# Kernel optimization log

Measured on AMD Instinct MI355X. Metric: run time of the kernel, lower is better.

The kernel has to match this reference:

```python
import jax, jax.numpy as jnp
import numpy as np

N, D, H = 8192, 256, 128
KEEP_RATIO = 0.5
TEMP = 1.0
COS_EPS = 1e-4  # torch CosineSimilarity eps
NEG = -9e15


def setup_inputs() -> dict:
    key = jax.random.key(0)
    k1, k2, k3, k4 = jax.random.split(key, 4)
    features = jax.random.normal(k1, (N, D), dtype=jnp.float32)
    adj = jax.random.randint(k2, (N, N), 0, 2, dtype=jnp.int32)
    # module init: Linear weights ~ N(0, 0.001)
    Wq = jax.random.normal(k3, (H, D), dtype=jnp.float32) * 0.001
    Wk = jax.random.normal(k4, (H, D), dtype=jnp.float32) * 0.001
    return {"features": features, "adj": adj, "Wq": Wq, "Wk": Wk}


def _cos_normalize(x):
    # torch cosine: x / max(||x||, eps)
    n = jnp.linalg.norm(x, axis=-1, keepdims=True)
    return x / jnp.maximum(n, COS_EPS)


def reference(features, adj, Wq, Wk):
    # projections [N, H]
    Qn = _cos_normalize(features @ Wq.T)
    Kn = _cos_normalize(features @ Wk.T)
    # raw_att[i, j] = cos(Wq f_j, Wk f_i)  -> [N, N]
    raw_att = Kn @ Qn.T
    att = jnp.where(adj > 0, raw_att, NEG) * TEMP
    att = jax.nn.softmax(att, axis=1)
    prop_fea = att @ features  # [N, D]
    # nodes with no neighbors keep their own features
    adj_mask = (jnp.sum(adj, axis=1) > 0).astype(features.dtype)[:, None]
    prop_fea = adj_mask * prop_fea + (1.0 - adj_mask) * features
    # gate=None branch: fixed keep_ratio mixing
    return (1.0 - KEEP_RATIO) * prop_fea + KEEP_RATIO * features
```

## Files before the change

kernel.cpp:

```cpp
#include <hip/hip_runtime.h>
#include <stdint.h>
#include <stddef.h>

#define NN 8192
#define DD 256
#define HH 128

typedef short bf16x8  __attribute__((ext_vector_type(8)));
typedef float f32x4   __attribute__((ext_vector_type(4)));
typedef float f32x16  __attribute__((ext_vector_type(16)));
typedef int   i32x4   __attribute__((ext_vector_type(4)));

static __device__ __forceinline__ short f2bf(float x){
  unsigned u = __float_as_uint(x);
  u = (u + 0x7FFFu + ((u >> 16) & 1u)) >> 16;
  return (short)(unsigned short)u;
}
static __device__ __forceinline__ bf16x8 cvt8(const float* p){
  f32x4 a = *(const f32x4*)p;
  f32x4 b = *(const f32x4*)(p + 4);
  bf16x8 o;
  o[0]=f2bf(a[0]); o[1]=f2bf(a[1]); o[2]=f2bf(a[2]); o[3]=f2bf(a[3]);
  o[4]=f2bf(b[0]); o[5]=f2bf(b[1]); o[6]=f2bf(b[2]); o[7]=f2bf(b[3]);
  return o;
}
static __device__ __forceinline__ bf16x8 ld16(const void* p){
  i32x4 v = *(const i32x4*)p;
  return __builtin_bit_cast(bf16x8, v);
}

__global__ __launch_bounds__(256) void k_prep(const float* __restrict__ f,
                                              const float* __restrict__ Wq,
                                              const float* __restrict__ Wk,
                                              unsigned short* __restrict__ ftf,
                                              unsigned short* __restrict__ Qnf,
                                              unsigned short* __restrict__ Kn){
  __shared__ unsigned short wb[128][40];
  int t = threadIdx.x, l = t & 63;
  {
    int fr = blockIdx.x * 4 + (t >> 6);
    int jt = fr >> 3, dt = fr & 7;
    int j = jt * 16 + (l >> 5) * 8, d = dt * 32 + (l & 31);
    bf16x8 o;
    #pragma unroll
    for (int e = 0; e < 8; ++e) o[e] = f2bf(f[(size_t)(j + e) * DD + d]);
    *(bf16x8*)(ftf + (size_t)fr * 512 + l * 8) = o;
  }
  if (blockIdx.x >= 128) return;
  int wave = t >> 6;
  int i0 = blockIdx.x * 64 + wave * 16;
  int lr = l & 15, lk = l >> 4;
  bf16x8 ka[8];
  #pragma unroll
  for (int ks = 0; ks < 8; ++ks)
    ka[ks] = cvt8(f + (size_t)(i0 + lr) * DD + ks * 32 + lk * 8);
  for (int pj = 0; pj < 2; ++pj){
    const float* W = pj ? Wk : Wq;
    f32x4 acc[8];
    #pragma unroll
    for (int n = 0; n < 8; ++n) acc[n] = (f32x4){0.f,0.f,0.f,0.f};
    for (int ks = 0; ks < 8; ++ks){
      __syncthreads();
      { int row = t >> 1, c0 = (t & 1) * 16;
        const float* wp = W + (size_t)row * DD + ks * 32 + c0;
        bf16x8 w0 = cvt8(wp), w1 = cvt8(wp + 8);
        *(bf16x8*)&wb[row][c0]     = w0;
        *(bf16x8*)&wb[row][c0 + 8] = w1; }
      __syncthreads();
      #pragma unroll
      for (int n = 0; n < 8; ++n){
        bf16x8 bb = ld16(&wb[n * 16 + lr][lk * 8]);
        acc[n] = __builtin_amdgcn_mfma_f32_16x16x32_bf16(ka[ks], bb, acc[n], 0, 0, 0);
      }
    }
    #pragma unroll
    for (int r = 0; r < 4; ++r){
      float n2 = 0.f;
      #pragma unroll
      for (int n = 0; n < 8; ++n){ float v = acc[n][r]; n2 += v * v; }
      n2 += __shfl_xor(n2, 1); n2 += __shfl_xor(n2, 2);
      n2 += __shfl_xor(n2, 4); n2 += __shfl_xor(n2, 8);
      float s = 1.f / fmaxf(sqrtf(n2), 1e-4f);
      int row = i0 + lk * 4 + r;
      #pragma unroll
      for (int n = 0; n < 8; ++n){
        short v = f2bf(acc[n][r] * s);
        if (pj){
          Kn[(size_t)row * HH + n * 16 + lr] = (unsigned short)v;
        } else {
          size_t off = ((size_t)(row >> 5) * 8 + n) * 512
                     + ((row & 31) + 32 * (lr >> 3)) * 8 + (lr & 7);
          Qnf[off] = (unsigned short)v;
        }
      }
    }
  }
}

__global__ __launch_bounds__(256, 2) void k_attn(
      const int* __restrict__ adj,
      const unsigned short* __restrict__ Qnf, const unsigned short* __restrict__ Kn,
      const unsigned short* __restrict__ ftf,
      float* __restrict__ num_p, float* __restrict__ den_p){
  __shared__ __attribute__((aligned(16))) char p_lds[8192];
  __shared__ __attribute__((aligned(16))) int adj_lds[2][64][64];
  int t = threadIdx.x, wave = t >> 6, l = t & 63;
  int lc = l & 31, h = l >> 5;
  int ig = wave >> 1, jg = wave & 1, wq = wave;
  int ib = blockIdx.x >> 2, js = blockIdx.x & 3;
  int i0 = ib * 64;
  int jbase = js * 2048;

  bf16x8 kb[8];
  { const unsigned short* kp = Kn + (size_t)(i0 + ig * 32 + lc) * HH + h * 8;
    #pragma unroll
    for (int hs = 0; hs < 8; ++hs) kb[hs] = ld16(kp + hs * 16); }

  f32x16 pv00, pv01, pv10, pv11;
  #pragma unroll
  for (int e = 0; e < 16; ++e){ pv00[e]=0.f; pv01[e]=0.f; pv10[e]=0.f; pv11[e]=0.f; }
  float dacc[16];
  #pragma unroll
  for (int r = 0; r < 16; ++r) dacc[r] = 0.f;

  int arow = wave * 16 + (l >> 4);
  int acol = (l & 15) * 4;

  #pragma unroll
  for (int k4 = 0; k4 < 4; ++k4){
    i32x4 v = __builtin_nontemporal_load(
        (const i32x4*)(adj + (size_t)(i0 + arow + k4 * 4) * NN + jbase + acol));
    *(i32x4*)&adj_lds[0][arow + k4 * 4][acol] = v;
  }
  __syncthreads();

  for (int s = 0; s < 32; ++s){
    int j0 = jbase + s * 64;
    int cur = s & 1, nxt = cur ^ 1;

    i32x4 av[4];
    if (s < 31){
      #pragma unroll
      for (int k4 = 0; k4 < 4; ++k4)
        av[k4] = __builtin_nontemporal_load(
            (const i32x4*)(adj + (size_t)(i0 + arow + k4 * 4) * NN + j0 + 64 + acol));
    }

    bf16x8 qv[8];
    { const unsigned short* qb = Qnf + ((size_t)((j0 + jg * 32) >> 5) * 8) * 512 + (size_t)l * 8;
      #pragma unroll
      for (int hs = 0; hs < 8; ++hs) qv[hs] = ld16(qb + hs * 512); }

    bf16x8 bv[8];
    { const unsigned short* fb = ftf + ((size_t)(j0 >> 4) * 8 + wq * 2) * 512 + (size_t)l * 8;
      #pragma unroll
      for (int ks = 0; ks < 4; ++ks){
        bv[ks * 2]     = ld16(fb + ks * 4096);
        bv[ks * 2 + 1] = ld16(fb + ks * 4096 + 512); } }

    f32x16 st;
    #pragma unroll
    for (int e = 0; e < 16; ++e) st[e] = 0.f;
    #pragma unroll
    for (int hs = 0; hs < 8; ++hs)
      st = __builtin_amdgcn_mfma_f32_32x32x16_bf16(kb[hs], qv[hs], st, 0, 0, 0);

    #pragma unroll
    for (int r = 0; r < 16; ++r){
      int row = ig * 32 + (r & 3) + 8 * (r >> 2) + 4 * h;
      int a = adj_lds[cur][row][jg * 32 + lc];
      float wv = (a > 0) ? __expf(st[r]) : 0.f;
      dacc[r] += wv;
      int byo = row * 128 + (((jg * 32 + lc) * 2) ^ ((row & 7) << 4));
      *(unsigned short*)(p_lds + byo) = (unsigned short)f2bf(wv);
    }
    __syncthreads();

    if (s < 31){
      #pragma unroll
      for (int k4 = 0; k4 < 4; ++k4)
        *(i32x4*)&adj_lds[nxt][arow + k4 * 4][acol] = av[k4];
    }

    #pragma unroll
    for (int ks = 0; ks < 4; ++ks){
      int ko = (ks * 32 + h * 16) ^ ((lc & 7) << 4);
      bf16x8 pa0 = ld16(p_lds + lc * 128 + ko);
      bf16x8 pa1 = ld16(p_lds + (32 + lc) * 128 + ko);
      pv00 = __builtin_amdgcn_mfma_f32_32x32x16_bf16(pa0, bv[ks*2],   pv00, 0,0,0);
      pv01 = __builtin_amdgcn_mfma_f32_32x32x16_bf16(pa0, bv[ks*2+1], pv01, 0,0,0);
      pv10 = __builtin_amdgcn_mfma_f32_32x32x16_bf16(pa1, bv[ks*2],   pv10, 0,0,0);
      pv11 = __builtin_amdgcn_mfma_f32_32x32x16_bf16(pa1, bv[ks*2+1], pv11, 0,0,0);
    }
    __syncthreads();
  }

  #pragma unroll
  for (int r = 0; r < 16; ++r){
    float v = dacc[r];
    v += __shfl_xor(v, 1); v += __shfl_xor(v, 2); v += __shfl_xor(v, 4);
    v += __shfl_xor(v, 8); v += __shfl_xor(v, 16);
    if (lc == 0){
      int i = i0 + ig * 32 + (r & 3) + 8 * (r >> 2) + 4 * h;
      den_p[(size_t)(js * 2 + jg) * NN + i] = v;
    }
  }
  float* np = num_p + (size_t)js * NN * DD;
  #pragma unroll
  for (int r = 0; r < 16; ++r){
    int i = i0 + (r & 3) + 8 * (r >> 2) + 4 * h;
    int d = wq * 64 + lc;
    np[(size_t)i * DD + d]             = pv00[r];
    np[(size_t)i * DD + d + 32]        = pv01[r];
    np[(size_t)(i + 32) * DD + d]      = pv10[r];
    np[(size_t)(i + 32) * DD + d + 32] = pv11[r];
  }
}

__global__ __launch_bounds__(256) void k_final(const float* __restrict__ num_p,
                                               const float* __restrict__ den_p,
                                               const float* __restrict__ f,
                                               float* __restrict__ out){
  int gid = blockIdx.x * 256 + threadIdx.x;
  int i = gid >> 6;
  f32x4 nv = (f32x4){0.f,0.f,0.f,0.f};
  float dv = 0.f;
  #pragma unroll
  for (int s = 0; s < 4; ++s)
    nv += *(const f32x4*)(num_p + (size_t)s * NN * DD + (size_t)gid * 4);
  #pragma unroll
  for (int s = 0; s < 8; ++s)
    dv += den_p[(size_t)s * NN + i];
  f32x4 fv = *(const f32x4*)(f + (size_t)gid * 4);
  f32x4 o;
  if (dv > 0.f){
    float inv = 0.5f / dv;
    o = nv * inv + fv * 0.5f;
  } else {
    o = fv;
  }
  *(f32x4*)(out + (size_t)gid * 4) = o;
}

extern "C" void kernel_launch(void* const* d_in, const int* in_sizes, int n_in,
                              void* d_out, int out_size, void* d_ws, size_t ws_size,
                              hipStream_t stream){
  (void)in_sizes; (void)n_in; (void)out_size;
  const float* feat = (const float*)d_in[0];
  const int*   adj  = (const int*)d_in[1];
  const float* Wq   = (const float*)d_in[2];
  const float* Wk   = (const float*)d_in[3];
  float* out = (float*)d_out;
  char* ws = (char*)d_ws;
  unsigned short* Qnf  = (unsigned short*)(ws);
  unsigned short* Kn   = (unsigned short*)(ws + (2u << 20));
  unsigned short* ftf  = (unsigned short*)(ws + (4u << 20));
  float*          num_p = (float*)(ws + (8u << 20));
  float*          den_p = (float*)(ws + (40u << 20));
  if (ws_size < (40u << 20) + 262144u) return;

  k_prep<<<1024, 256, 0, stream>>>(feat, Wq, Wk, ftf, Qnf, Kn);
  k_attn<<<512, 256, 0, stream>>>(adj, Qnf, Kn, ftf, num_p, den_p);
  k_final<<<2048, 256, 0, stream>>>(num_p, den_p, feat, out);
}
```

Baseline: 193.2 us.

## Fuse prep, attention and final kernels into one cooperative persistent kernel

Merges the three kernels into one phase-switched kernel launched cooperatively with 512 blocks, separated by grid-wide syncs. The prep and final phases are remapped so that each block covers more work to fit the 512-block grid. The aim is to remove two kernel launch gaps and their tail effects. In exchange it adds grid-sync cost and requires 512 blocks to be co-resident (two per CU on 256 CUs); if the cooperative launch fails, it falls back to three launches.

```diff
diff --git a/kernel.cpp b/kernel.cpp
--- a/kernel.cpp
+++ b/kernel.cpp
@@ -1,10 +1,13 @@
 #include <hip/hip_runtime.h>
+#include <hip/hip_cooperative_groups.h>
 #include <stdint.h>
 #include <stddef.h>
 
 #define NN 8192
 #define DD 256
 #define HH 128
+
+namespace cg = cooperative_groups;
 
 typedef short bf16x8  __attribute__((ext_vector_type(8)));
 typedef float f32x4   __attribute__((ext_vector_type(4)));
@@ -29,217 +32,220 @@
   return __builtin_bit_cast(bf16x8, v);
 }
 
-__global__ __launch_bounds__(256) void k_prep(const float* __restrict__ f,
-                                              const float* __restrict__ Wq,
-                                              const float* __restrict__ Wk,
-                                              unsigned short* __restrict__ ftf,
-                                              unsigned short* __restrict__ Qnf,
-                                              unsigned short* __restrict__ Kn){
+__global__ __launch_bounds__(256, 2) void k_mega(
+    const float* __restrict__ f, const int* __restrict__ adj,
+    const float* __restrict__ Wq, const float* __restrict__ Wk,
+    unsigned short* __restrict__ ftf, unsigned short* __restrict__ Qnf,
+    unsigned short* __restrict__ Kn,
+    float* __restrict__ num_p, float* __restrict__ den_p,
+    float* __restrict__ out, int phase)
+{
   __shared__ unsigned short wb[128][40];
-  int t = threadIdx.x, l = t & 63;
-  {
-    int fr = blockIdx.x * 4 + (t >> 6);
-    int jt = fr >> 3, dt = fr & 7;
-    int j = jt * 16 + (l >> 5) * 8, d = dt * 32 + (l & 31);
-    bf16x8 o;
-    #pragma unroll
-    for (int e = 0; e < 8; ++e) o[e] = f2bf(f[(size_t)(j + e) * DD + d]);
-    *(bf16x8*)(ftf + (size_t)fr * 512 + l * 8) = o;
-  }
-  if (blockIdx.x >= 128) return;
-  int wave = t >> 6;
-  int i0 = blockIdx.x * 64 + wave * 16;
-  int lr = l & 15, lk = l >> 4;
-  bf16x8 ka[8];
-  #pragma unroll
-  for (int ks = 0; ks < 8; ++ks)
-    ka[ks] = cvt8(f + (size_t)(i0 + lr) * DD + ks * 32 + lk * 8);
-  for (int pj = 0; pj < 2; ++pj){
-    const float* W = pj ? Wk : Wq;
-    f32x4 acc[8];
-    #pragma unroll
-    for (int n = 0; n < 8; ++n) acc[n] = (f32x4){0.f,0.f,0.f,0.f};
-    for (int ks = 0; ks < 8; ++ks){
-      __syncthreads();
-      { int row = t >> 1, c0 = (t & 1) * 16;
-        const float* wp = W + (size_t)row * DD + ks * 32 + c0;
-        bf16x8 w0 = cvt8(wp), w1 = cvt8(wp + 8);
-        *(bf16x8*)&wb[row][c0]     = w0;
-        *(bf16x8*)&wb[row][c0 + 8] = w1; }
-      __syncthreads();
-      #pragma unroll
-      for (int n = 0; n < 8; ++n){
-        bf16x8 bb = ld16(&wb[n * 16 + lr][lk * 8]);
-        acc[n] = __builtin_amdgcn_mfma_f32_16x16x32_bf16(ka[ks], bb, acc[n], 0, 0, 0);
-      }
-    }
-    #pragma unroll
-    for (int r = 0; r < 4; ++r){
-      float n2 = 0.f;
-      #pragma unroll
-      for (int n = 0; n < 8; ++n){ float v = acc[n][r]; n2 += v * v; }
-      n2 += __shfl_xor(n2, 1); n2 += __shfl_xor(n2, 2);
-      n2 += __shfl_xor(n2, 4); n2 += __shfl_xor(n2, 8);
-      float s = 1.f / fmaxf(sqrtf(n2), 1e-4f);
-      int row = i0 + lk * 4 + r;
-      #pragma unroll
-      for (int n = 0; n < 8; ++n){
-        short v = f2bf(acc[n][r] * s);
-        if (pj){
-          Kn[(size_t)row * HH + n * 16 + lr] = (unsigned short)v;
-        } else {
-          size_t off = ((size_t)(row >> 5) * 8 + n) * 512
-                     + ((row & 31) + 32 * (lr >> 3)) * 8 + (lr & 7);
-          Qnf[off] = (unsigned short)v;
-        }
-      }
-    }
-  }
-}
-
-__global__ __launch_bounds__(256, 2) void k_attn(
-      const int* __restrict__ adj,
-      const unsigned short* __restrict__ Qnf, const unsigned short* __restrict__ Kn,
-      const unsigned short* __restrict__ ftf,
-      float* __restrict__ num_p, float* __restrict__ den_p){
   __shared__ __attribute__((aligned(16))) char p_lds[8192];
   __shared__ __attribute__((aligned(16))) int adj_lds[2][64][64];
-  int t = threadIdx.x, wave = t >> 6, l = t & 63;
-  int lc = l & 31, h = l >> 5;
-  int ig = wave >> 1, jg = wave & 1, wq = wave;
-  int ib = blockIdx.x >> 2, js = blockIdx.x & 3;
-  int i0 = ib * 64;
-  int jbase = js * 2048;
-
-  bf16x8 kb[8];
-  { const unsigned short* kp = Kn + (size_t)(i0 + ig * 32 + lc) * HH + h * 8;
-    #pragma unroll
-    for (int hs = 0; hs < 8; ++hs) kb[hs] = ld16(kp + hs * 16); }
-
-  f32x16 pv00, pv01, pv10, pv11;
+  int bid = blockIdx.x, t = threadIdx.x, wave = t >> 6, l = t & 63;
+
+  if (phase <= 0){
+    #pragma unroll
+    for (int sub = 0; sub < 2; ++sub){
+      int fr = bid * 8 + wave * 2 + sub;
+      int jt = fr >> 3, dt = fr & 7;
+      int j = jt * 16 + (l >> 5) * 8, d = dt * 32 + (l & 31);
+      bf16x8 o;
+      #pragma unroll
+      for (int e = 0; e < 8; ++e) o[e] = f2bf(f[(size_t)(j + e) * DD + d]);
+      *(bf16x8*)(ftf + (size_t)fr * 512 + l * 8) = o;
+    }
+    if (bid < 128){
+      int i0 = bid * 64 + wave * 16;
+      int lr = l & 15, lk = l >> 4;
+      bf16x8 ka[8];
+      #pragma unroll
+      for (int ks = 0; ks < 8; ++ks)
+        ka[ks] = cvt8(f + (size_t)(i0 + lr) * DD + ks * 32 + lk * 8);
+      for (int pj = 0; pj < 2; ++pj){
+        const float* W = pj ? Wk : Wq;
+        f32x4 acc[8];
+        #pragma unroll
+        for (int n = 0; n < 8; ++n) acc[n] = (f32x4){0.f,0.f,0.f,0.f};
+        for (int ks = 0; ks < 8; ++ks){
+          __syncthreads();
+          { int row = t >> 1, c0 = (t & 1) * 16;
+            const float* wp = W + (size_t)row * DD + ks * 32 + c0;
+            bf16x8 w0 = cvt8(wp), w1 = cvt8(wp + 8);
+            *(bf16x8*)&wb[row][c0]     = w0;
+            *(bf16x8*)&wb[row][c0 + 8] = w1; }
+          __syncthreads();
+          #pragma unroll
+          for (int n = 0; n < 8; ++n){
+            bf16x8 bb = ld16(&wb[n * 16 + lr][lk * 8]);
+            acc[n] = __builtin_amdgcn_mfma_f32_16x16x32_bf16(ka[ks], bb, acc[n], 0, 0, 0);
+          }
+        }
+        #pragma unroll
+        for (int r = 0; r < 4; ++r){
+          float n2 = 0.f;
+          #pragma unroll
+          for (int n = 0; n < 8; ++n){ float v = acc[n][r]; n2 += v * v; }
+          n2 += __shfl_xor(n2, 1); n2 += __shfl_xor(n2, 2);
+          n2 += __shfl_xor(n2, 4); n2 += __shfl_xor(n2, 8);
+          float s = 1.f / fmaxf(sqrtf(n2), 1e-4f);
+          int row = i0 + lk * 4 + r;
+          #pragma unroll
+          for (int n = 0; n < 8; ++n){
+            short v = f2bf(acc[n][r] * s);
+            if (pj){
+              Kn[(size_t)row * HH + n * 16 + lr] = (unsigned short)v;
+            } else {
+              size_t off = ((size_t)(row >> 5) * 8 + n) * 512
+                         + ((row & 31) + 32 * (lr >> 3)) * 8 + (lr & 7);
+              Qnf[off] = (unsigned short)v;
+            }
+          }
+        }
+      }
+    }
+  }
+  if (phase == 0) return;
+  if (phase < 0) cg::this_grid().sync();
+
+  if (phase <= 1){
+    int lc = l & 31, h = l >> 5;
+    int ig = wave >> 1, jg = wave & 1, wq = wave;
+    int ib = bid >> 2, js = bid & 3;
+    int i0 = ib * 64;
+    int jbase = js * 2048;
+
+    bf16x8 kb[8];
+    { const unsigned short* kp = Kn + (size_t)(i0 + ig * 32 + lc) * HH + h * 8;
+      #pragma unroll
+      for (int hs = 0; hs < 8; ++hs) kb[hs] = ld16(kp + hs * 16); }
+
+    f32x16 pv00, pv01, pv10, pv11;
+    #pragma unroll
+    for (int e = 0; e < 16; ++e){ pv00[e]=0.f; pv01[e]=0.f; pv10[e]=0.f; pv11[e]=0.f; }
+    float dacc[16];
+    #pragma unroll
+    for (int r = 0; r < 16; ++r) dacc[r] = 0.f;
+
+    int arow = wave * 16 + (l >> 4);
+    int acol = (l & 15) * 4;
+
+    #pragma unroll
+    for (int k4 = 0; k4 < 4; ++k4){
+      i32x4 v = __builtin_nontemporal_load(
+          (const i32x4*)(adj + (size_t)(i0 + arow + k4 * 4) * NN + jbase + acol));
+      *(i32x4*)&adj_lds[0][arow + k4 * 4][acol] = v;
+    }
+    __syncthreads();
+
+    for (int s = 0; s < 32; ++s){
+      int j0 = jbase + s * 64;
+      int cur = s & 1, nxt = cur ^ 1;
+
+      i32x4 av[4];
+      if (s < 31){
+        #pragma unroll
+        for (int k4 = 0; k4 < 4; ++k4)
+          av[k4] = __builtin_nontemporal_load(
+              (const i32x4*)(adj + (size_t)(i0 + arow + k4 * 4) * NN + j0 + 64 + acol));
+      }
+
+      bf16x8 qv[8];
+      { const unsigned short* qb = Qnf + ((size_t)((j0 + jg * 32) >> 5) * 8) * 512 + (size_t)l * 8;
+        #pragma unroll
+        for (int hs = 0; hs < 8; ++hs) qv[hs] = ld16(qb + hs * 512); }
+
+      bf16x8 bv[8];
+      { const unsigned short* fb = ftf + ((size_t)(j0 >> 4) * 8 + wq * 2) * 512 + (size_t)l * 8;
+        #pragma unroll
+        for (int ks = 0; ks < 4; ++ks){
+          bv[ks * 2]     = ld16(fb + ks * 4096);
+          bv[ks * 2 + 1] = ld16(fb + ks * 4096 + 512); } }
+
+      f32x16 st;
+      #pragma unroll
+      for (int e = 0; e < 16; ++e) st[e] = 0.f;
+      #pragma unroll
+      for (int hs = 0; hs < 8; ++hs)
+        st = __builtin_amdgcn_mfma_f32_32x32x16_bf16(kb[hs], qv[hs], st, 0, 0, 0);
+
+      #pragma unroll
+      for (int r = 0; r < 16; ++r){
+        int row = ig * 32 + (r & 3) + 8 * (r >> 2) + 4 * h;
+        int a = adj_lds[cur][row][jg * 32 + lc];
+        float wv = (a > 0) ? __expf(st[r]) : 0.f;
+        dacc[r] += wv;
+        int byo = row * 128 + (((jg * 32 + lc) * 2) ^ ((row & 7) << 4));
+        *(unsigned short*)(p_lds + byo) = (unsigned short)f2bf(wv);
+      }
+      __syncthreads();
+
+      if (s < 31){
+        #pragma unroll
+        for (int k4 = 0; k4 < 4; ++k4)
+          *(i32x4*)&adj_lds[nxt][arow + k4 * 4][acol] = av[k4];
+      }
+
+      #pragma unroll
+      for (int ks = 0; ks < 4; ++ks){
+        int ko = (ks * 32 + h * 16) ^ ((lc & 7) << 4);
+        bf16x8 pa0 = ld16(p_lds + lc * 128 + ko);
+        bf16x8 pa1 = ld16(p_lds + (32 + lc) * 128 + ko);
+        pv00 = __builtin_amdgcn_mfma_f32_32x32x16_bf16(pa0, bv[ks*2],   pv00, 0,0,0);
+        pv01 = __builtin_amdgcn_mfma_f32_32x32x16_bf16(pa0, bv[ks*2+1], pv01, 0,0,0);
+        pv10 = __builtin_amdgcn_mfma_f32_32x32x16_bf16(pa1, bv[ks*2],   pv10, 0,0,0);
+        pv11 = __builtin_amdgcn_mfma_f32_32x32x16_bf16(pa1, bv[ks*2+1], pv11, 0,0,0);
+      }
+      __syncthreads();
+    }
+
+    #pragma unroll
+    for (int r = 0; r < 16; ++r){
+      float v = dacc[r];
+      v += __shfl_xor(v, 1); v += __shfl_xor(v, 2); v += __shfl_xor(v, 4);
+      v += __shfl_xor(v, 8); v += __shfl_xor(v, 16);
+      if (lc == 0){
+        int i = i0 + ig * 32 + (r & 3) + 8 * (r >> 2) + 4 * h;
+        den_p[(size_t)(js * 2 + jg) * NN + i] = v;
+      }
+    }
+    float* np = num_p + (size_t)js * NN * DD;
+    #pragma unroll
+    for (int r = 0; r < 16; ++r){
+      int i = i0 + (r & 3) + 8 * (r >> 2) + 4 * h;
+      int d = wq * 64 + lc;
+      np[(size_t)i * DD + d]             = pv00[r];
+      np[(size_t)i * DD + d + 32]        = pv01[r];
+      np[(size_t)(i + 32) * DD + d]      = pv10[r];
+      np[(size_t)(i + 32) * DD + d + 32] = pv11[r];
+    }
+  }
+  if (phase == 1) return;
+  if (phase < 0) cg::this_grid().sync();
+
   #pragma unroll
-  for (int e = 0; e < 16; ++e){ pv00[e]=0.f; pv01[e]=0.f; pv10[e]=0.f; pv11[e]=0.f; }
-  float dacc[16];
-  #pragma unroll
-  for (int r = 0; r < 16; ++r) dacc[r] = 0.f;
-
-  int arow = wave * 16 + (l >> 4);
-  int acol = (l & 15) * 4;
-
-  #pragma unroll
-  for (int k4 = 0; k4 < 4; ++k4){
-    i32x4 v = __builtin_nontemporal_load(
-        (const i32x4*)(adj + (size_t)(i0 + arow + k4 * 4) * NN + jbase + acol));
-    *(i32x4*)&adj_lds[0][arow + k4 * 4][acol] = v;
-  }
-  __syncthreads();
-
-  for (int s = 0; s < 32; ++s){
-    int j0 = jbase + s * 64;
-    int cur = s & 1, nxt = cur ^ 1;
-
-    i32x4 av[4];
-    if (s < 31){
-      #pragma unroll
-      for (int k4 = 0; k4 < 4; ++k4)
-        av[k4] = __builtin_nontemporal_load(
-            (const i32x4*)(adj + (size_t)(i0 + arow + k4 * 4) * NN + j0 + 64 + acol));
-    }
-
-    bf16x8 qv[8];
-    { const unsigned short* qb = Qnf + ((size_t)((j0 + jg * 32) >> 5) * 8) * 512 + (size_t)l * 8;
-      #pragma unroll
-      for (int hs = 0; hs < 8; ++hs) qv[hs] = ld16(qb + hs * 512); }
-
-    bf16x8 bv[8];
-    { const unsigned short* fb = ftf + ((size_t)(j0 >> 4) * 8 + wq * 2) * 512 + (size_t)l * 8;
-      #pragma unroll
-      for (int ks = 0; ks < 4; ++ks){
-        bv[ks * 2]     = ld16(fb + ks * 4096);
-        bv[ks * 2 + 1] = ld16(fb + ks * 4096 + 512); } }
-
-    f32x16 st;
-    #pragma unroll
-    for (int e = 0; e < 16; ++e) st[e] = 0.f;
-    #pragma unroll
-    for (int hs = 0; hs < 8; ++hs)
-      st = __builtin_amdgcn_mfma_f32_32x32x16_bf16(kb[hs], qv[hs], st, 0, 0, 0);
-
-    #pragma unroll
-    for (int r = 0; r < 16; ++r){
-      int row = ig * 32 + (r & 3) + 8 * (r >> 2) + 4 * h;
-      int a = adj_lds[cur][row][jg * 32 + lc];
-      float wv = (a > 0) ? __expf(st[r]) : 0.f;
-      dacc[r] += wv;
-      int byo = row * 128 + (((jg * 32 + lc) * 2) ^ ((row & 7) << 4));
-      *(unsigned short*)(p_lds + byo) = (unsigned short)f2bf(wv);
-    }
-    __syncthreads();
-
-    if (s < 31){
-      #pragma unroll
-      for (int k4 = 0; k4 < 4; ++k4)
-        *(i32x4*)&adj_lds[nxt][arow + k4 * 4][acol] = av[k4];
-    }
-
-    #pragma unroll
-    for (int ks = 0; ks < 4; ++ks){
-      int ko = (ks * 32 + h * 16) ^ ((lc & 7) << 4);
-      bf16x8 pa0 = ld16(p_lds + lc * 128 + ko);
-      bf16x8 pa1 = ld16(p_lds + (32 + lc) * 128 + ko);
-      pv00 = __builtin_amdgcn_mfma_f32_32x32x16_bf16(pa0, bv[ks*2],   pv00, 0,0,0);
-      pv01 = __builtin_amdgcn_mfma_f32_32x32x16_bf16(pa0, bv[ks*2+1], pv01, 0,0,0);
-      pv10 = __builtin_amdgcn_mfma_f32_32x32x16_bf16(pa1, bv[ks*2],   pv10, 0,0,0);
-      pv11 = __builtin_amdgcn_mfma_f32_32x32x16_bf16(pa1, bv[ks*2+1], pv11, 0,0,0);
-    }
-    __syncthreads();
-  }
-
-  #pragma unroll
-  for (int r = 0; r < 16; ++r){
-    float v = dacc[r];
-    v += __shfl_xor(v, 1); v += __shfl_xor(v, 2); v += __shfl_xor(v, 4);
-    v += __shfl_xor(v, 8); v += __shfl_xor(v, 16);
-    if (lc == 0){
-      int i = i0 + ig * 32 + (r & 3) + 8 * (r >> 2) + 4 * h;
-      den_p[(size_t)(js * 2 + jg) * NN + i] = v;
-    }
-  }
-  float* np = num_p + (size_t)js * NN * DD;
-  #pragma unroll
-  for (int r = 0; r < 16; ++r){
-    int i = i0 + (r & 3) + 8 * (r >> 2) + 4 * h;
-    int d = wq * 64 + lc;
-    np[(size_t)i * DD + d]             = pv00[r];
-    np[(size_t)i * DD + d + 32]        = pv01[r];
-    np[(size_t)(i + 32) * DD + d]      = pv10[r];
-    np[(size_t)(i + 32) * DD + d + 32] = pv11[r];
-  }
-}
-
-__global__ __launch_bounds__(256) void k_final(const float* __restrict__ num_p,
-                                               const float* __restrict__ den_p,
-                                               const float* __restrict__ f,
-                                               float* __restrict__ out){
-  int gid = blockIdx.x * 256 + threadIdx.x;
-  int i = gid >> 6;
-  f32x4 nv = (f32x4){0.f,0.f,0.f,0.f};
-  float dv = 0.f;
-  #pragma unroll
-  for (int s = 0; s < 4; ++s)
-    nv += *(const f32x4*)(num_p + (size_t)s * NN * DD + (size_t)gid * 4);
-  #pragma unroll
-  for (int s = 0; s < 8; ++s)
-    dv += den_p[(size_t)s * NN + i];
-  f32x4 fv = *(const f32x4*)(f + (size_t)gid * 4);
-  f32x4 o;
-  if (dv > 0.f){
-    float inv = 0.5f / dv;
-    o = nv * inv + fv * 0.5f;
-  } else {
-    o = fv;
-  }
-  *(f32x4*)(out + (size_t)gid * 4) = o;
+  for (int it = 0; it < 4; ++it){
+    int g = bid * 1024 + it * 256 + t;
+    int i = g >> 6;
+    f32x4 nv = (f32x4){0.f,0.f,0.f,0.f};
+    #pragma unroll
+    for (int s2 = 0; s2 < 4; ++s2)
+      nv += *(const f32x4*)(num_p + (size_t)s2 * NN * DD + (size_t)g * 4);
+    float dv = 0.f;
+    #pragma unroll
+    for (int s2 = 0; s2 < 8; ++s2)
+      dv += den_p[(size_t)s2 * NN + i];
+    f32x4 fv = *(const f32x4*)(f + (size_t)g * 4);
+    f32x4 o;
+    if (dv > 0.f){
+      float inv = 0.5f / dv;
+      o = nv * inv + fv * 0.5f;
+    } else {
+      o = fv;
+    }
+    *(f32x4*)(out + (size_t)g * 4) = o;
+  }
 }
 
 extern "C" void kernel_launch(void* const* d_in, const int* in_sizes, int n_in,
@@ -252,14 +258,23 @@
   const float* Wk   = (const float*)d_in[3];
   float* out = (float*)d_out;
   char* ws = (char*)d_ws;
-  unsigned short* Qnf  = (unsigned short*)(ws);
-  unsigned short* Kn   = (unsigned short*)(ws + (2u << 20));
-  unsigned short* ftf  = (unsigned short*)(ws + (4u << 20));
+  unsigned short* Qnf   = (unsigned short*)(ws);
+  unsigned short* Kn    = (unsigned short*)(ws + (2u << 20));
+  unsigned short* ftf   = (unsigned short*)(ws + (4u << 20));
   float*          num_p = (float*)(ws + (8u << 20));
   float*          den_p = (float*)(ws + (40u << 20));
   if (ws_size < (40u << 20) + 262144u) return;
 
-  k_prep<<<1024, 256, 0, stream>>>(feat, Wq, Wk, ftf, Qnf, Kn);
-  k_attn<<<512, 256, 0, stream>>>(adj, Qnf, Kn, ftf, num_p, den_p);
-  k_final<<<2048, 256, 0, stream>>>(num_p, den_p, feat, out);
-}
+  int ph = -1;
+  void* args[] = {(void*)&feat, (void*)&adj, (void*)&Wq, (void*)&Wk,
+                  (void*)&ftf, (void*)&Qnf, (void*)&Kn,
+                  (void*)&num_p, (void*)&den_p, (void*)&out, (void*)&ph};
+  hipError_t e = hipLaunchCooperativeKernel((const void*)k_mega, dim3(512), dim3(256),
+                                            args, 0, stream);
+  if (e != hipSuccess){
+    (void)hipGetLastError();
+    k_mega<<<512, 256, 0, stream>>>(feat, adj, Wq, Wk, ftf, Qnf, Kn, num_p, den_p, out, 0);
+    k_mega<<<512, 256, 0, stream>>>(feat, adj, Wq, Wk, ftf, Qnf, Kn, num_p, den_p, out, 1);
+    k_mega<<<512, 256, 0, stream>>>(feat, adj, Wq, Wk, ftf, Qnf, Kn, num_p, den_p, out, 2);
+  }
+}
```

After: 263.0 us. 1.36x slower.
